# Kernel tuning notes

Hardware: AMD Instinct MI355X
Metric: run time of the kernel (lower is better)

Reference implementation:

```python
import jax, jax.numpy as jnp
import numpy as np


def _gcn_conv(x, W, b, src, dst, n):
    # PyG GCNConv: add self-loops, symmetric normalization deg^{-1/2} A deg^{-1/2},
    # linear transform, scatter-add aggregation, bias.
    h = x @ W  # [N, H]
    # degree including self-loop (count of dst occurrences + 1)
    deg = jnp.zeros((n,), h.dtype).at[dst].add(1.0) + 1.0
    dinv = jax.lax.rsqrt(deg)  # deg^{-1/2}
    edge_norm = (dinv[src] * dinv[dst])[:, None]  # [E, 1]
    agg = jax.ops.segment_sum(h[src] * edge_norm, dst, num_segments=n)  # [N, H]
    # self-loop contribution: norm = dinv[i]*dinv[i]
    return agg + h * (dinv * dinv)[:, None] + b


def setup_inputs() -> dict:
    N, E, F_IN, HID, OUT = 100000, 1600000, 128, 128, 64
    key = jax.random.key(0)
    ks = jax.random.split(key, 8)
    x = jax.random.normal(ks[0], (N, F_IN), dtype=jnp.float32)
    edge_index = jax.random.randint(ks[1], (2, E), 0, N, dtype=jnp.int32)
    s1 = 1.0 / np.sqrt(F_IN)
    s2 = 1.0 / np.sqrt(HID)
    W1 = jax.random.uniform(ks[2], (F_IN, HID), jnp.float32, -s1, s1)
    b1 = jax.random.uniform(ks[3], (HID,), jnp.float32, -s1, s1)
    W2 = jax.random.uniform(ks[4], (HID, HID), jnp.float32, -s2, s2)
    b2 = jax.random.uniform(ks[5], (HID,), jnp.float32, -s2, s2)
    W_out = jax.random.uniform(ks[6], (HID, OUT), jnp.float32, -s2, s2)
    b_out = jax.random.uniform(ks[7], (OUT,), jnp.float32, -s2, s2)
    return {"x": x, "edge_index": edge_index, "W1": W1, "b1": b1,
            "W2": W2, "b2": b2, "W_out": W_out, "b_out": b_out}


def reference(x, edge_index, W1, b1, W2, b2, W_out, b_out):
    n = x.shape[0]
    src, dst = edge_index[0], edge_index[1]
    h = _gcn_conv(x, W1, b1, src, dst, n)
    h = jax.nn.relu(h)
    # F.dropout(training=self.training): identity in eval mode
    h = _gcn_conv(h, W2, b2, src, dst, n)
    h = jax.nn.relu(h)
    logits = h @ W_out + b_out
    return jax.nn.log_softmax(logits, axis=1)
```

## Files before the change

### kernel.cpp

```cpp
#include <hip/hip_runtime.h>
#include <hip/hip_bf16.h>


#define FEAT 128
#define OUTF 64
#define BSH 7
#define BNODES (1 << BSH)
#define SCHUNK_SH 12
#define SCHUNK (1 << SCHUNK_SH)
#define NREP 8
#define GDEPTH 16

typedef __attribute__((ext_vector_type(8))) short short8;
typedef __attribute__((ext_vector_type(4))) float f32x4;

__device__ __forceinline__ unsigned short bf16_rn(float f) {
    unsigned int u = __float_as_uint(f);
    u += 0x7FFFu + ((u >> 16) & 1u);
    return (unsigned short)(u >> 16);
}
__device__ __forceinline__ float bf16_lo(unsigned int u) { return __uint_as_float(u << 16); }
__device__ __forceinline__ float bf16_hi(unsigned int u) { return __uint_as_float(u & 0xFFFF0000u); }

__global__ __launch_bounds__(256) void bincount8_kernel(
        const int* __restrict__ dst, int* __restrict__ bcnt8, int E, int NB) {
    __shared__ int h[8192];
    int t = threadIdx.x;
    int nb8 = NB * NREP;
    for (int i = t; i < nb8; i += 256) h[i] = 0;
    __syncthreads();
    int stride = gridDim.x * 256;
    for (int e = blockIdx.x * 256 + t; e < E; e += stride) {
        int rep = (e >> SCHUNK_SH) & (NREP - 1);
        atomicAdd(&h[((dst[e] >> BSH) << 3) | rep], 1);
    }
    __syncthreads();
    for (int i = t; i < nb8; i += 256)
        if (h[i]) atomicAdd(&bcnt8[i], h[i]);
}

__global__ __launch_bounds__(1024) void bucket_scan8_kernel(
        const int* __restrict__ bcnt8, int* __restrict__ bcur8,
        int* __restrict__ bbase, int NB, int E) {
    int t = threadIdx.x;
    int nb8 = NB * NREP;
    int base = t * 8;
    int v[8];
    #pragma unroll
    for (int i = 0; i < 8; ++i) v[i] = (base + i < nb8) ? bcnt8[base + i] : 0;
    int local = 0;
    #pragma unroll
    for (int i = 0; i < 8; ++i) local += v[i];
    int lane = t & 63, wv = t >> 6;
    int x = local;
    #pragma unroll
    for (int o = 1; o < 64; o <<= 1) {
        int y = __shfl_up(x, o);
        if (lane >= o) x += y;
    }
    __shared__ int wsum[16];
    if (lane == 63) wsum[wv] = x;
    __syncthreads();
    int woff = 0;
    for (int i = 0; i < wv; ++i) woff += wsum[i];
    int run = woff + x - local;
    #pragma unroll
    for (int i = 0; i < 8; ++i) {
        int g = base + i;
        if (g < nb8) {
            bcur8[g] = run;
            if ((g & (NREP - 1)) == 0) bbase[g >> 3] = run;
        }
        run += v[i];
    }
    if (t == 0) bbase[NB] = E;
}

__global__ __launch_bounds__(256) void bin_scatter_kernel(
        const int* __restrict__ src, const int* __restrict__ dst,
        int* __restrict__ bcur8, unsigned int* __restrict__ staged,
        int E, int NB) {
    __shared__ int lcnt[1024];
    __shared__ int lbase[1024];
    int t = threadIdx.x;
    int rep = blockIdx.x & (NREP - 1);
    int e0 = blockIdx.x << SCHUNK_SH;
    int e1 = min(e0 + SCHUNK, E);
    for (int i = t; i < NB; i += 256) lcnt[i] = 0;
    __syncthreads();
    for (int e = e0 + t; e < e1; e += 256)
        atomicAdd(&lcnt[dst[e] >> BSH], 1);
    __syncthreads();
    for (int i = t; i < NB; i += 256) {
        int c = lcnt[i];
        lbase[i] = c ? atomicAdd(&bcur8[(i << 3) | rep], c) : 0;
        lcnt[i] = 0;
    }
    __syncthreads();
    for (int e = e0 + t; e < e1; e += 256) {
        int s = src[e], d = dst[e];
        int b = d >> BSH, dl = d & (BNODES - 1);
        int pos = lbase[b] + atomicAdd(&lcnt[b], 1);
        staged[pos] = (unsigned int)s | ((unsigned int)dl << 25);
    }
}

__global__ __launch_bounds__(256) void bucket_place_kernel(
        const unsigned int* __restrict__ staged, const int* __restrict__ bbase,
        int* __restrict__ row_ptr, float* __restrict__ dinv,
        int* __restrict__ csr_src, int N, int E) {
    int b = blockIdx.x;
    int t = threadIdx.x;
    int base = bbase[b], end = bbase[b + 1];
    __shared__ int cnt[BNODES];
    __shared__ int cur[BNODES];
    __shared__ int wsum2[2];
    if (t < BNODES) cnt[t] = 0;
    __syncthreads();
    for (int i = base + t; i < end; i += 256)
        atomicAdd(&cnt[staged[i] >> 25], 1);
    __syncthreads();

    bool act = t < BNODES;
    int v = act ? cnt[t] : 0;
    int lane = t & 63, wv = t >> 6;
    int x = v;
    #pragma unroll
    for (int o = 1; o < 64; o <<= 1) {
        int y = __shfl_up(x, o);
        if (lane >= o) x += y;
    }
    if (lane == 63 && wv == 0) wsum2[0] = x;
    __syncthreads();
    if (act) {
        int excl = x - v + (wv == 1 ? wsum2[0] : 0);
        int gnode = b * BNODES + t;
        int rp = base + excl;
        cur[t] = rp;
        if (gnode < N) {
            row_ptr[gnode] = rp;
            dinv[gnode] = rsqrtf((float)v + 1.0f);
        }
    }
    __syncthreads();
    for (int i = base + t; i < end; i += 256) {
        unsigned int u = staged[i];
        int dl = u >> 25;
        int p = atomicAdd(&cur[dl], 1);
        csr_src[p] = (int)(u & 0x1FFFFFFu);
    }
    if (b == 0 && t == 0) row_ptr[N] = E;
}

__global__ __launch_bounds__(256) void convw_kernel(
        const float* __restrict__ W1, const float* __restrict__ W2,
        const float* __restrict__ Wout,
        __hip_bfloat16* __restrict__ W1t, __hip_bfloat16* __restrict__ W2t,
        __hip_bfloat16* __restrict__ WoutT) {
    int idx = blockIdx.x * 256 + threadIdx.x;
    if (idx < 2 * FEAT * FEAT) {
        int which = idx >> 14;
        int r = idx & (FEAT * FEAT - 1);
        int n = r >> 7, k = r & 127;
        const float* W = which ? W2 : W1;
        unsigned short* Wt = (unsigned short*)(which ? W2t : W1t);
        Wt[r] = bf16_rn(W[k * FEAT + n]);
    } else if (idx < 2 * FEAT * FEAT + OUTF * FEAT) {
        int r = idx - 2 * FEAT * FEAT;
        int n = r >> 7, k = r & 127;
        ((unsigned short*)WoutT)[r] = bf16_rn(Wout[k * OUTF + n]);
    }
}

template <bool IN_FP32>
__global__ __launch_bounds__(256) void mfma_gemm_kernel(
        const void* __restrict__ Xv, const __hip_bfloat16* __restrict__ Wt,
        const float* __restrict__ dinv, __hip_bfloat16* __restrict__ Y, int N) {
    __shared__ short Ws[FEAT][136];
    int t = threadIdx.x;
    for (int i = t; i < FEAT * 16; i += 256) {
        int n = i >> 4, c = i & 15;
        *(uint4*)&Ws[n][c * 8] = *(const uint4*)((const unsigned short*)Wt + n * FEAT + c * 8);
    }
    __syncthreads();

    int wave = t >> 6, lane = t & 63;
    int m = lane & 15, quad = lane >> 4;
    int rbase = (blockIdx.x * 4 + wave) * 16;
    if (rbase >= N) return;
    int row = rbase + m;
    bool rok = row < N;

    f32x4 acc[8];
    #pragma unroll
    for (int nt = 0; nt < 8; ++nt) acc[nt] = (f32x4){0.f, 0.f, 0.f, 0.f};

    #pragma unroll
    for (int ks = 0; ks < 4; ++ks) {
        short8 a;
        if (IN_FP32) {
            const float* X = (const float*)Xv;
            float xs[8];
            if (rok) {
                float4 x0 = *(const float4*)(X + (size_t)row * FEAT + ks * 32 + quad * 8);
                float4 x1 = *(const float4*)(X + (size_t)row * FEAT + ks * 32 + quad * 8 + 4);
                xs[0] = x0.x; xs[1] = x0.y; xs[2] = x0.z; xs[3] = x0.w;
                xs[4] = x1.x; xs[5] = x1.y; xs[6] = x1.z; xs[7] = x1.w;
            } else {
                #pragma unroll
                for (int j = 0; j < 8; ++j) xs[j] = 0.f;
            }
            #pragma unroll
            for (int j = 0; j < 8; ++j) a[j] = (short)bf16_rn(xs[j]);
        } else {
            const unsigned short* X = (const unsigned short*)Xv;
            if (rok)
                a = *(const short8*)(X + (size_t)row * FEAT + ks * 32 + quad * 8);
            else {
                #pragma unroll
                for (int j = 0; j < 8; ++j) a[j] = 0;
            }
        }
        #pragma unroll
        for (int nt = 0; nt < 8; ++nt) {
            short8 bfr = *(const short8*)&Ws[nt * 16 + m][ks * 32 + quad * 8];
            acc[nt] = __builtin_amdgcn_mfma_f32_16x16x32_bf16(a, bfr, acc[nt], 0, 0, 0);
        }
    }

    float dr[4];
    #pragma unroll
    for (int r = 0; r < 4; ++r) {
        int ro = rbase + quad * 4 + r;
        dr[r] = (ro < N) ? dinv[ro] : 0.f;
    }
    unsigned short* Yo = (unsigned short*)Y;
    #pragma unroll
    for (int nt = 0; nt < 8; ++nt) {
        #pragma unroll
        for (int r = 0; r < 4; ++r) {
            int ro = rbase + quad * 4 + r;
            if (ro < N)
                Yo[(size_t)ro * FEAT + nt * 16 + m] = bf16_rn(acc[nt][r] * dr[r]);
        }
    }
}

__global__ __launch_bounds__(256, 4) void gather_kernel(
        const int* __restrict__ row_ptr, const int* __restrict__ csr_src,
        const float* __restrict__ dinv, const __hip_bfloat16* __restrict__ Hs,
        const float* __restrict__ bias, __hip_bfloat16* __restrict__ A, int N) {
    int t = threadIdx.x;
    int lane = t & 63;
    int wave = t >> 6;
    int grp = lane >> 4;
    int fl = lane & 15;
    int node = blockIdx.x * 16 + wave * 4 + grp;
    bool nok = node < N;
    int nd = nok ? node : 0;

    const char* Hb = (const char*)Hs;
    unsigned foff = (unsigned)fl << 4;

    uint4 hu = *(const uint4*)(Hb + (((unsigned)nd << 8) + foff));
    float di = dinv[nd];
    float4 b0 = ((const float4*)bias)[fl * 2];
    float4 b1 = ((const float4*)bias)[fl * 2 + 1];

    float acc[8];
    #pragma unroll
    for (int i = 0; i < 8; ++i) acc[i] = 0.f;

    int j = row_ptr[nd], end = row_ptr[nd + 1];

    for (; j + GDEPTH <= end; j += GDEPTH) {
        unsigned off[GDEPTH];
        #pragma unroll
        for (int k = 0; k < GDEPTH; ++k)
            off[k] = ((unsigned)csr_src[j + k] << 8) + foff;
        uint4 u[GDEPTH];
        #pragma unroll
        for (int k = 0; k < GDEPTH; ++k)
            u[k] = *(const uint4*)(Hb + off[k]);
        #pragma unroll
        for (int k = 0; k < GDEPTH; ++k) {
            acc[0] += bf16_lo(u[k].x); acc[1] += bf16_hi(u[k].x);
            acc[2] += bf16_lo(u[k].y); acc[3] += bf16_hi(u[k].y);
            acc[4] += bf16_lo(u[k].z); acc[5] += bf16_hi(u[k].z);
            acc[6] += bf16_lo(u[k].w); acc[7] += bf16_hi(u[k].w);
        }
    }
    if (j < end) {
        int m = end - j;
        unsigned off[GDEPTH];
        #pragma unroll
        for (int k = 0; k < GDEPTH; ++k)
            off[k] = ((unsigned)csr_src[j + (k < m ? k : 0)] << 8) + foff;
        uint4 u[GDEPTH];
        #pragma unroll
        for (int k = 0; k < GDEPTH; ++k)
            u[k] = *(const uint4*)(Hb + off[k]);
        #pragma unroll
        for (int k = 0; k < GDEPTH; ++k) {
            if (k < m) {
                acc[0] += bf16_lo(u[k].x); acc[1] += bf16_hi(u[k].x);
                acc[2] += bf16_lo(u[k].y); acc[3] += bf16_hi(u[k].y);
                acc[4] += bf16_lo(u[k].z); acc[5] += bf16_hi(u[k].z);
                acc[6] += bf16_lo(u[k].w); acc[7] += bf16_hi(u[k].w);
            }
        }
    }

    acc[0] += bf16_lo(hu.x); acc[1] += bf16_hi(hu.x);
    acc[2] += bf16_lo(hu.y); acc[3] += bf16_hi(hu.y);
    acc[4] += bf16_lo(hu.z); acc[5] += bf16_hi(hu.z);
    acc[6] += bf16_lo(hu.w); acc[7] += bf16_hi(hu.w);

    float v0 = fmaxf(di * acc[0] + b0.x, 0.f);
    float v1 = fmaxf(di * acc[1] + b0.y, 0.f);
    float v2 = fmaxf(di * acc[2] + b0.z, 0.f);
    float v3 = fmaxf(di * acc[3] + b0.w, 0.f);
    float v4 = fmaxf(di * acc[4] + b1.x, 0.f);
    float v5 = fmaxf(di * acc[5] + b1.y, 0.f);
    float v6 = fmaxf(di * acc[6] + b1.z, 0.f);
    float v7 = fmaxf(di * acc[7] + b1.w, 0.f);

    uint4 o;
    o.x = (unsigned int)bf16_rn(v0) | ((unsigned int)bf16_rn(v1) << 16);
    o.y = (unsigned int)bf16_rn(v2) | ((unsigned int)bf16_rn(v3) << 16);
    o.z = (unsigned int)bf16_rn(v4) | ((unsigned int)bf16_rn(v5) << 16);
    o.w = (unsigned int)bf16_rn(v6) | ((unsigned int)bf16_rn(v7) << 16);
    if (nok)
        ((uint4*)A)[(size_t)node * 16 + fl] = o;
}

__global__ __launch_bounds__(256) void final_mfma_kernel(
        const __hip_bfloat16* __restrict__ H, const __hip_bfloat16* __restrict__ WoutT,
        const float* __restrict__ bout, float* __restrict__ out, int N) {
    __shared__ short Ws[OUTF][136];
    int t = threadIdx.x;
    for (int i = t; i < OUTF * 16; i += 256) {
        int n = i >> 4, c = i & 15;
        *(uint4*)&Ws[n][c * 8] = *(const uint4*)((const unsigned short*)WoutT + n * FEAT + c * 8);
    }
    __syncthreads();

    int wave = t >> 6, lane = t & 63;
    int m = lane & 15, quad = lane >> 4;
    int rbase = blockIdx.x * 64 + wave * 16;
    if (rbase >= N) return;
    int row = rbase + m;
    bool rok = row < N;

    f32x4 acc[4];
    #pragma unroll
    for (int nt = 0; nt < 4; ++nt) acc[nt] = (f32x4){0.f, 0.f, 0.f, 0.f};

    const unsigned short* Hu = (const unsigned short*)H;
    #pragma unroll
    for (int ks = 0; ks < 4; ++ks) {
        short8 a;
        if (rok)
            a = *(const short8*)(Hu + (size_t)row * FEAT + ks * 32 + quad * 8);
        else {
            #pragma unroll
            for (int j = 0; j < 8; ++j) a[j] = 0;
        }
        #pragma unroll
        for (int nt = 0; nt < 4; ++nt) {
            short8 bfr = *(const short8*)&Ws[nt * 16 + m][ks * 32 + quad * 8];
            acc[nt] = __builtin_amdgcn_mfma_f32_16x16x32_bf16(a, bfr, acc[nt], 0, 0, 0);
        }
    }

    float bj[4];
    #pragma unroll
    for (int nt = 0; nt < 4; ++nt) bj[nt] = bout[nt * 16 + m];

    #pragma unroll
    for (int r = 0; r < 4; ++r) {
        int ro = rbase + quad * 4 + r;
        if (ro >= N) continue;
        float v0 = acc[0][r] + bj[0];
        float v1 = acc[1][r] + bj[1];
        float v2 = acc[2][r] + bj[2];
        float v3 = acc[3][r] + bj[3];
        float mx = fmaxf(fmaxf(v0, v1), fmaxf(v2, v3));
        #pragma unroll
        for (int o = 1; o <= 8; o <<= 1) mx = fmaxf(mx, __shfl_xor(mx, o));
        float s = __expf(v0 - mx) + __expf(v1 - mx) + __expf(v2 - mx) + __expf(v3 - mx);
        #pragma unroll
        for (int o = 1; o <= 8; o <<= 1) s += __shfl_xor(s, o);
        float ls = mx + __logf(s);
        float* op = out + (size_t)ro * OUTF + m;
        op[0]  = v0 - ls;
        op[16] = v1 - ls;
        op[32] = v2 - ls;
        op[48] = v3 - ls;
    }
}

extern "C" void kernel_launch(void* const* d_in, const int* in_sizes, int n_in,
                              void* d_out, int out_size, void* d_ws, size_t ws_size,
                              hipStream_t stream) {
    const float* x    = (const float*)d_in[0];
    const int*   ei   = (const int*)  d_in[1];
    const float* W1   = (const float*)d_in[2];
    const float* b1   = (const float*)d_in[3];
    const float* W2   = (const float*)d_in[4];
    const float* b2   = (const float*)d_in[5];
    const float* Wout = (const float*)d_in[6];
    const float* bout = (const float*)d_in[7];
    float* out = (float*)d_out;

    int N = in_sizes[0] / FEAT;
    int E = in_sizes[1] / 2;
    const int* srcp = ei;
    const int* dstp = ei + E;
    int NB = (N + BNODES - 1) >> BSH;

    char* ws = (char*)d_ws;
    __hip_bfloat16* Bh   = (__hip_bfloat16*)ws;
    __hip_bfloat16* Ba   = Bh + (size_t)N * FEAT;
    __hip_bfloat16* W1t  = Ba + (size_t)N * FEAT;
    __hip_bfloat16* W2t  = W1t + FEAT * FEAT;
    __hip_bfloat16* WoutT = W2t + FEAT * FEAT;
    float* dinv    = (float*)(WoutT + OUTF * FEAT);
    int*   rowp    = (int*)(dinv + N);
    int*   bcnt8   = rowp + N + 1;
    int*   bcur8   = bcnt8 + 8192;
    int*   bbase   = bcur8 + 8192;
    unsigned int* staged = (unsigned int*)(bbase + 1032);
    int*   csrsrc  = (int*)(staged + E);

    hipMemsetAsync(bcnt8, 0, (size_t)NB * NREP * sizeof(int), stream);
    bincount8_kernel<<<256, 256, 0, stream>>>(dstp, bcnt8, E, NB);
    bucket_scan8_kernel<<<1, 1024, 0, stream>>>(bcnt8, bcur8, bbase, NB, E);
    bin_scatter_kernel<<<(E + SCHUNK - 1) / SCHUNK, 256, 0, stream>>>(
        srcp, dstp, bcur8, staged, E, NB);
    bucket_place_kernel<<<NB, 256, 0, stream>>>(staged, bbase, rowp, dinv, csrsrc, N, E);
    convw_kernel<<<(2 * FEAT * FEAT + OUTF * FEAT + 255) / 256, 256, 0, stream>>>(
        W1, W2, Wout, W1t, W2t, WoutT);

    int ggrid = (N + 63) / 64;
    int agrid = (N + 15) / 16;

    mfma_gemm_kernel<true><<<ggrid, 256, 0, stream>>>(x, W1t, dinv, Bh, N);
    gather_kernel<<<agrid, 256, 0, stream>>>(rowp, csrsrc, dinv, Bh, b1, Ba, N);

    mfma_gemm_kernel<false><<<ggrid, 256, 0, stream>>>(Ba, W2t, dinv, Bh, N);
    gather_kernel<<<agrid, 256, 0, stream>>>(rowp, csrsrc, dinv, Bh, b2, Ba, N);

    final_mfma_kernel<<<(N + 63) / 64, 256, 0, stream>>>(Ba, WoutT, bout, out, N);
}
```

Baseline: 339.6 us.

## Fuse next-layer GEMM and final log-softmax into gather kernel epilogues

The gather/aggregate kernel now stages its 16 aggregated rows in LDS and runs the following dense GEMM in-block with MFMA. In the first layer it multiplies by W2 and scales by dinv to produce the next layer's pre-aggregation input. In the second layer it applies W_out, the bias and log-softmax. This removes two separate kernel launches and the round trip of intermediate activations through global memory. In exchange, each block loads the whole weight matrix into LDS, which is redundant work across many small blocks. LDS use also grows (about 39KB for layer 1), which may reduce occupancy of the latency-bound gather. In layer 2 only one wave does the epilogue.

```diff
diff --git a/kernel.cpp b/kernel.cpp
--- a/kernel.cpp
+++ b/kernel.cpp
@@ -246,11 +246,22 @@
     }
 }
 
-__global__ __launch_bounds__(256, 4) void gather_kernel(
+template <int EPI>
+__global__ __launch_bounds__(256, 4) void gather_fused_kernel(
         const int* __restrict__ row_ptr, const int* __restrict__ csr_src,
         const float* __restrict__ dinv, const __hip_bfloat16* __restrict__ Hs,
-        const float* __restrict__ bias, __hip_bfloat16* __restrict__ A, int N) {
-    int t = threadIdx.x;
+        const float* __restrict__ bias, const __hip_bfloat16* __restrict__ Wt,
+        const float* __restrict__ bvec, void* __restrict__ outp, int N) {
+    constexpr int WR = (EPI == 1) ? FEAT : OUTF;
+    __shared__ short Ws[WR][136];
+    __shared__ short As[16][136];
+
+    int t = threadIdx.x;
+    for (int i = t; i < WR * 16; i += 256) {
+        int n = i >> 4, c = i & 15;
+        *(uint4*)&Ws[n][c * 8] = *(const uint4*)((const unsigned short*)Wt + n * FEAT + c * 8);
+    }
+
     int lane = t & 63;
     int wave = t >> 6;
     int grp = lane >> 4;
@@ -291,18 +302,18 @@
         }
     }
     if (j < end) {
-        int m = end - j;
+        int mm = end - j;
         unsigned off[GDEPTH];
         #pragma unroll
         for (int k = 0; k < GDEPTH; ++k)
-            off[k] = ((unsigned)csr_src[j + (k < m ? k : 0)] << 8) + foff;
+            off[k] = ((unsigned)csr_src[j + (k < mm ? k : 0)] << 8) + foff;
         uint4 u[GDEPTH];
         #pragma unroll
         for (int k = 0; k < GDEPTH; ++k)
             u[k] = *(const uint4*)(Hb + off[k]);
         #pragma unroll
         for (int k = 0; k < GDEPTH; ++k) {
-            if (k < m) {
+            if (k < mm) {
                 acc[0] += bf16_lo(u[k].x); acc[1] += bf16_hi(u[k].x);
                 acc[2] += bf16_lo(u[k].y); acc[3] += bf16_hi(u[k].y);
                 acc[4] += bf16_lo(u[k].z); acc[5] += bf16_hi(u[k].z);
@@ -330,73 +341,79 @@
     o.y = (unsigned int)bf16_rn(v2) | ((unsigned int)bf16_rn(v3) << 16);
     o.z = (unsigned int)bf16_rn(v4) | ((unsigned int)bf16_rn(v5) << 16);
     o.w = (unsigned int)bf16_rn(v6) | ((unsigned int)bf16_rn(v7) << 16);
-    if (nok)
-        ((uint4*)A)[(size_t)node * 16 + fl] = o;
-}
-
-__global__ __launch_bounds__(256) void final_mfma_kernel(
-        const __hip_bfloat16* __restrict__ H, const __hip_bfloat16* __restrict__ WoutT,
-        const float* __restrict__ bout, float* __restrict__ out, int N) {
-    __shared__ short Ws[OUTF][136];
-    int t = threadIdx.x;
-    for (int i = t; i < OUTF * 16; i += 256) {
-        int n = i >> 4, c = i & 15;
-        *(uint4*)&Ws[n][c * 8] = *(const uint4*)((const unsigned short*)WoutT + n * FEAT + c * 8);
-    }
-    __syncthreads();
-
-    int wave = t >> 6, lane = t & 63;
+
+    *(uint4*)&As[wave * 4 + grp][fl * 8] = o;
+    __syncthreads();
+
     int m = lane & 15, quad = lane >> 4;
-    int rbase = blockIdx.x * 64 + wave * 16;
-    if (rbase >= N) return;
-    int row = rbase + m;
-    bool rok = row < N;
-
-    f32x4 acc[4];
-    #pragma unroll
-    for (int nt = 0; nt < 4; ++nt) acc[nt] = (f32x4){0.f, 0.f, 0.f, 0.f};
-
-    const unsigned short* Hu = (const unsigned short*)H;
-    #pragma unroll
-    for (int ks = 0; ks < 4; ++ks) {
-        short8 a;
-        if (rok)
-            a = *(const short8*)(Hu + (size_t)row * FEAT + ks * 32 + quad * 8);
-        else {
-            #pragma unroll
-            for (int j = 0; j < 8; ++j) a[j] = 0;
-        }
-        #pragma unroll
-        for (int nt = 0; nt < 4; ++nt) {
-            short8 bfr = *(const short8*)&Ws[nt * 16 + m][ks * 32 + quad * 8];
-            acc[nt] = __builtin_amdgcn_mfma_f32_16x16x32_bf16(a, bfr, acc[nt], 0, 0, 0);
-        }
-    }
-
-    float bj[4];
-    #pragma unroll
-    for (int nt = 0; nt < 4; ++nt) bj[nt] = bout[nt * 16 + m];
-
-    #pragma unroll
-    for (int r = 0; r < 4; ++r) {
-        int ro = rbase + quad * 4 + r;
-        if (ro >= N) continue;
-        float v0 = acc[0][r] + bj[0];
-        float v1 = acc[1][r] + bj[1];
-        float v2 = acc[2][r] + bj[2];
-        float v3 = acc[3][r] + bj[3];
-        float mx = fmaxf(fmaxf(v0, v1), fmaxf(v2, v3));
-        #pragma unroll
-        for (int o = 1; o <= 8; o <<= 1) mx = fmaxf(mx, __shfl_xor(mx, o));
-        float s = __expf(v0 - mx) + __expf(v1 - mx) + __expf(v2 - mx) + __expf(v3 - mx);
-        #pragma unroll
-        for (int o = 1; o <= 8; o <<= 1) s += __shfl_xor(s, o);
-        float ls = mx + __logf(s);
-        float* op = out + (size_t)ro * OUTF + m;
-        op[0]  = v0 - ls;
-        op[16] = v1 - ls;
-        op[32] = v2 - ls;
-        op[48] = v3 - ls;
+    int rbase0 = blockIdx.x * 16;
+
+    if (EPI == 1) {
+        f32x4 acc2[2];
+        #pragma unroll
+        for (int n2 = 0; n2 < 2; ++n2) acc2[n2] = (f32x4){0.f, 0.f, 0.f, 0.f};
+        #pragma unroll
+        for (int ks = 0; ks < 4; ++ks) {
+            short8 a = *(const short8*)&As[m][ks * 32 + quad * 8];
+            #pragma unroll
+            for (int n2 = 0; n2 < 2; ++n2) {
+                int nt = wave * 2 + n2;
+                short8 bfr = *(const short8*)&Ws[nt * 16 + m][ks * 32 + quad * 8];
+                acc2[n2] = __builtin_amdgcn_mfma_f32_16x16x32_bf16(a, bfr, acc2[n2], 0, 0, 0);
+            }
+        }
+        unsigned short* Yo = (unsigned short*)outp;
+        #pragma unroll
+        for (int r = 0; r < 4; ++r) {
+            int ro = rbase0 + quad * 4 + r;
+            if (ro < N) {
+                float dr = dinv[ro];
+                #pragma unroll
+                for (int n2 = 0; n2 < 2; ++n2)
+                    Yo[(size_t)ro * FEAT + (wave * 2 + n2) * 16 + m] =
+                        bf16_rn(acc2[n2][r] * dr);
+            }
+        }
+    } else {
+        if (wave == 0) {
+            f32x4 acc4[4];
+            #pragma unroll
+            for (int nt = 0; nt < 4; ++nt) acc4[nt] = (f32x4){0.f, 0.f, 0.f, 0.f};
+            #pragma unroll
+            for (int ks = 0; ks < 4; ++ks) {
+                short8 a = *(const short8*)&As[m][ks * 32 + quad * 8];
+                #pragma unroll
+                for (int nt = 0; nt < 4; ++nt) {
+                    short8 bfr = *(const short8*)&Ws[nt * 16 + m][ks * 32 + quad * 8];
+                    acc4[nt] = __builtin_amdgcn_mfma_f32_16x16x32_bf16(a, bfr, acc4[nt], 0, 0, 0);
+                }
+            }
+            float bj[4];
+            #pragma unroll
+            for (int nt = 0; nt < 4; ++nt) bj[nt] = bvec[nt * 16 + m];
+            float* out = (float*)outp;
+            #pragma unroll
+            for (int r = 0; r < 4; ++r) {
+                int ro = rbase0 + quad * 4 + r;
+                if (ro >= N) continue;
+                float w0 = acc4[0][r] + bj[0];
+                float w1 = acc4[1][r] + bj[1];
+                float w2 = acc4[2][r] + bj[2];
+                float w3 = acc4[3][r] + bj[3];
+                float mx = fmaxf(fmaxf(w0, w1), fmaxf(w2, w3));
+                #pragma unroll
+                for (int os = 1; os <= 8; os <<= 1) mx = fmaxf(mx, __shfl_xor(mx, os));
+                float s = __expf(w0 - mx) + __expf(w1 - mx) + __expf(w2 - mx) + __expf(w3 - mx);
+                #pragma unroll
+                for (int os = 1; os <= 8; os <<= 1) s += __shfl_xor(s, os);
+                float ls = mx + __logf(s);
+                float* op = out + (size_t)ro * OUTF + m;
+                op[0]  = w0 - ls;
+                op[16] = w1 - ls;
+                op[32] = w2 - ls;
+                op[48] = w3 - ls;
+            }
+        }
     }
 }
 
@@ -446,10 +463,10 @@
     int agrid = (N + 15) / 16;
 
     mfma_gemm_kernel<true><<<ggrid, 256, 0, stream>>>(x, W1t, dinv, Bh, N);
-    gather_kernel<<<agrid, 256, 0, stream>>>(rowp, csrsrc, dinv, Bh, b1, Ba, N);
-
-    mfma_gemm_kernel<false><<<ggrid, 256, 0, stream>>>(Ba, W2t, dinv, Bh, N);
-    gather_kernel<<<agrid, 256, 0, stream>>>(rowp, csrsrc, dinv, Bh, b2, Ba, N);
-
-    final_mfma_kernel<<<(N + 63) / 64, 256, 0, stream>>>(Ba, WoutT, bout, out, N);
-}
+
+    gather_fused_kernel<1><<<agrid, 256, 0, stream>>>(
+        rowp, csrsrc, dinv, Bh, b1, W2t, nullptr, Ba, N);
+
+    gather_fused_kernel<2><<<agrid, 256, 0, stream>>>(
+        rowp, csrsrc, dinv, Ba, b2, WoutT, bout, out, N);
+}
```

New measurement: 323.6 us. 1.05x faster.
